# Kernel tuning notes

Hardware: AMD Instinct MI355X
Metric: run time of the kernel (lower is better)

Reference implementation:

```python
import jax, jax.numpy as jnp
import numpy as np

N_EMBD = 1024
N_HEAD = 16
HEAD_DIM = N_EMBD // N_HEAD


def setup_inputs() -> dict:
    key = jax.random.key(0)
    ks = jax.random.split(key, 5)
    scale = 0.02
    x = jax.random.normal(ks[0], (2, 2048, N_EMBD), dtype=jnp.float32)
    w_attn = jax.random.normal(ks[1], (N_EMBD, 3 * N_EMBD), dtype=jnp.float32) * scale
    b_attn = jax.random.normal(ks[2], (3 * N_EMBD,), dtype=jnp.float32) * scale
    w_proj = jax.random.normal(ks[3], (N_EMBD, N_EMBD), dtype=jnp.float32) * scale
    b_proj = jax.random.normal(ks[4], (N_EMBD,), dtype=jnp.float32) * scale
    return {"x": x, "w_attn": w_attn, "b_attn": b_attn, "w_proj": w_proj, "b_proj": b_proj}


def reference(x, w_attn, b_attn, w_proj, b_proj):
    B, T, C = x.shape
    qkv = x @ w_attn + b_attn  # [B,T,3C]
    q, k, v = jnp.split(qkv, 3, axis=-1)
    # [B, H, T, D]
    q = q.reshape(B, T, N_HEAD, HEAD_DIM).transpose(0, 2, 1, 3)
    k = k.reshape(B, T, N_HEAD, HEAD_DIM).transpose(0, 2, 1, 3)
    v = v.reshape(B, T, N_HEAD, HEAD_DIM).transpose(0, 2, 1, 3)
    att = jnp.einsum("bhqd,bhkd->bhqk", q, k) * (1.0 / np.sqrt(HEAD_DIM))
    causal = jnp.tril(jnp.ones((T, T), dtype=bool))
    att = jnp.where(causal[None, None], att, jnp.float32(-jnp.inf))
    att = jax.nn.softmax(att, axis=-1)
    y = jnp.einsum("bhqk,bhkd->bhqd", att, v)  # [B,H,T,D]
    y = y.transpose(0, 2, 1, 3).reshape(B, T, C)
    return y @ w_proj + b_proj
```

## Files before the change

kernel.cpp:

```cpp
#include <hip/hip_runtime.h>
#include <stdint.h>

#define SEQ   2048
#define EMBD  1024
#define M_ROWS 4096

typedef unsigned short u16;
typedef unsigned int u32;
typedef __attribute__((ext_vector_type(8))) short bf16x8;
typedef __attribute__((ext_vector_type(4))) float f32x4;

__device__ __forceinline__ u16 f2b(float f) {
  u32 x = __float_as_uint(f);
  return (u16)((x + 0x7FFFu + ((x >> 16) & 1u)) >> 16);
}

#define AS1(p) ((const __attribute__((address_space(1))) void*)(uintptr_t)(p))
#define AS3(p) ((__attribute__((address_space(3))) void*)(uintptr_t)(p))

__global__ __launch_bounds__(256) void cvt_f32_bf16(
    const float* __restrict__ in, u16* __restrict__ out, int n8) {
  int i = blockIdx.x * 256 + threadIdx.x;
  if (i >= n8) return;
  const float4* p = (const float4*)in + 2 * (size_t)i;
  float4 a = p[0], b = p[1];
  uint4 o;
  o.x = (u32)f2b(a.x) | ((u32)f2b(a.y) << 16);
  o.y = (u32)f2b(a.z) | ((u32)f2b(a.w) << 16);
  o.z = (u32)f2b(b.x) | ((u32)f2b(b.y) << 16);
  o.w = (u32)f2b(b.z) | ((u32)f2b(b.w) << 16);
  ((uint4*)out)[i] = o;
}

__global__ __launch_bounds__(256) void transpose_cvt(
    const float* __restrict__ w, u16* __restrict__ wt, int K, int N) {
  __shared__ float t[64][65];
  const int n0 = blockIdx.x * 64, k0 = blockIdx.y * 64;
  const int c = threadIdx.x & 63, r4 = threadIdx.x >> 6;
#pragma unroll
  for (int j = 0; j < 16; ++j) {
    const int r = j * 4 + r4;
    t[c][r] = w[(size_t)(k0 + r) * N + n0 + c];
  }
  __syncthreads();
#pragma unroll
  for (int j = 0; j < 16; ++j) {
    const int nr = j * 4 + r4;
    wt[(size_t)(n0 + nr) * K + k0 + c] = f2b(t[nr][c]);
  }
}

template <bool OUT_BF16>
__global__ __launch_bounds__(256) void gemm_kmajor(
    const u16* __restrict__ A, const u16* __restrict__ Bt,
    const float* __restrict__ bias, void* __restrict__ outp,
    int M, int N, int K, int nbx) {
  __shared__ __align__(16) u16 As[128 * 32];
  __shared__ __align__(16) u16 Bs[128 * 32];

  const int nwg = gridDim.x;
  const int qq = nwg >> 3, rr = nwg & 7;
  const int xcd = blockIdx.x & 7, off = blockIdx.x >> 3;
  const int wgid = (xcd < rr ? xcd * (qq + 1) : rr * (qq + 1) + (xcd - rr) * qq) + off;
  const int bx = wgid % nbx, by = wgid / nbx;
  const int row0 = by * 128, col0 = bx * 128;

  const int tid = threadIdx.x;
  const int w = tid >> 6, lane = tid & 63;
  const int wrow = (w >> 1) * 64, wcol = (w & 1) * 64;

  f32x4 acc[4][4];
#pragma unroll
  for (int a = 0; a < 4; ++a)
#pragma unroll
    for (int b = 0; b < 4; ++b)
#pragma unroll
      for (int e = 0; e < 4; ++e) acc[a][b][e] = 0.f;

  const size_t Kb = (size_t)K * 2;

  for (int k0 = 0; k0 < K; k0 += 32) {
#pragma unroll
    for (int c = 0; c < 4; ++c) {
      const int ch = w * 4 + c;
      const int i = ch & 7;
      const int rloc = i * 16 + (lane >> 2);
      const int kb = ((lane & 3) * 16) ^ ((rloc & 3) << 4);
      const char* src;
      char* dst;
      if (ch < 8) {
        src = (const char*)A + (size_t)(row0 + rloc) * Kb + k0 * 2 + kb;
        dst = (char*)As + i * 1024;
      } else {
        src = (const char*)Bt + (size_t)(col0 + rloc) * Kb + k0 * 2 + kb;
        dst = (char*)Bs + i * 1024;
      }
      __builtin_amdgcn_global_load_lds(AS1(src), AS3(dst), 16, 0, 0);
    }
    __syncthreads();

    bf16x8 af[4], bf[4];
#pragma unroll
    for (int rb = 0; rb < 4; ++rb) {
      const int rl = wrow + rb * 16 + (lane & 15);
      const int kb2 = ((lane >> 4) * 16) ^ ((rl & 3) << 4);
      af[rb] = *(const bf16x8*)((const char*)As + rl * 64 + kb2);
    }
#pragma unroll
    for (int cb = 0; cb < 4; ++cb) {
      const int rl = wcol + cb * 16 + (lane & 15);
      const int kb2 = ((lane >> 4) * 16) ^ ((rl & 3) << 4);
      bf[cb] = *(const bf16x8*)((const char*)Bs + rl * 64 + kb2);
    }
#pragma unroll
    for (int rb = 0; rb < 4; ++rb)
#pragma unroll
      for (int cb = 0; cb < 4; ++cb)
        acc[rb][cb] = __builtin_amdgcn_mfma_f32_16x16x32_bf16(
            af[rb], bf[cb], acc[rb][cb], 0, 0, 0);
    __syncthreads();
  }

#pragma unroll
  for (int cb = 0; cb < 4; ++cb) {
    const int colg = col0 + wcol + cb * 16 + (lane & 15);
    const float bv = bias[colg];
#pragma unroll
    for (int rb = 0; rb < 4; ++rb) {
#pragma unroll
      for (int i = 0; i < 4; ++i) {
        const int rowg = row0 + wrow + rb * 16 + (lane >> 4) * 4 + i;
        const float v = acc[rb][cb][i] + bv;
        if (OUT_BF16) {
          const u32 hv = f2b(v);
          const u32 pv = (u32)__shfl_xor((int)hv, 1);
          if (!(lane & 1))
            *(u32*)((u16*)outp + (size_t)rowg * N + colg) = hv | (pv << 16);
        } else {
          ((float*)outp)[(size_t)rowg * N + colg] = v;
        }
      }
    }
  }
}

__global__ __launch_bounds__(256) void attn_mfma(
    const u16* __restrict__ qkvb, u16* __restrict__ yb) {
  __shared__ __align__(16) u16 Ks[64 * 64];
  __shared__ __align__(16) u16 Vt[64 * 64];
  __shared__ __align__(16) u16 Ps[4][16 * 64];

  const int bx = blockIdx.x;
  const int qt = 31 - (bx >> 5);
  const int bh = bx & 31;
  const int bb = bh >> 4, h = bh & 15;

  const int tid = threadIdx.x;
  const int w = tid >> 6, lane = tid & 63;

  const size_t rowb = 3072 * 2;
  const char* base = (const char*)qkvb + (size_t)bb * SEQ * rowb;
  const int qoffb = h * 128;
  const int koffb = EMBD * 2 + h * 128;
  const int voffb = 2 * EMBD * 2 + h * 128;

  bf16x8 qf[2];
  {
    const int qrow = qt * 64 + w * 16 + (lane & 15);
    const char* qp = base + (size_t)qrow * rowb + qoffb + (lane >> 4) * 16;
    qf[0] = *(const bf16x8*)(qp);
    qf[1] = *(const bf16x8*)(qp + 64);
  }

  float mreg[4], lreg[4];
  f32x4 of[4];
#pragma unroll
  for (int i = 0; i < 4; ++i) {
    mreg[i] = -1e30f;
    lreg[i] = 0.f;
#pragma unroll
    for (int e = 0; e < 4; ++e) of[i][e] = 0.f;
  }

  const int vkv = tid & 63, vdb = tid >> 6;

  for (int kt = 0; kt <= qt; ++kt) {
#pragma unroll
    for (int c = 0; c < 2; ++c) {
      const int i = w * 2 + c;
      const int kv = i * 8 + (lane >> 3);
      const int db = ((lane & 7) * 16) ^ ((kv & 7) << 4);
      const char* src = base + (size_t)(kt * 64 + kv) * rowb + koffb + db;
      __builtin_amdgcn_global_load_lds(AS1(src), AS3((char*)Ks + i * 1024), 16, 0, 0);
    }
    {
      const char* vp = base + (size_t)(kt * 64 + vkv) * rowb + voffb + vdb * 32;
      union { uint4 q4[2]; u16 hh[16]; } vv;
      vv.q4[0] = *(const uint4*)vp;
      vv.q4[1] = *(const uint4*)(vp + 16);
#pragma unroll
      for (int e = 0; e < 16; ++e) {
        const int d = vdb * 16 + e;
        Vt[d * 64 + (vkv ^ ((d & 7) << 3))] = vv.hh[e];
      }
    }
    __syncthreads();

    f32x4 s[4];
#pragma unroll
    for (int cb = 0; cb < 4; ++cb)
#pragma unroll
      for (int e = 0; e < 4; ++e) s[cb][e] = 0.f;
#pragma unroll
    for (int cb = 0; cb < 4; ++cb) {
      const int kv = cb * 16 + (lane & 15);
      const int swz = (kv & 7) << 4;
      const char* kp = (const char*)Ks + kv * 128;
      bf16x8 kf0 = *(const bf16x8*)(kp + (((lane >> 4) * 16) ^ swz));
      bf16x8 kf1 = *(const bf16x8*)(kp + ((64 + (lane >> 4) * 16) ^ swz));
      s[cb] = __builtin_amdgcn_mfma_f32_16x16x32_bf16(qf[0], kf0, s[cb], 0, 0, 0);
      s[cb] = __builtin_amdgcn_mfma_f32_16x16x32_bf16(qf[1], kf1, s[cb], 0, 0, 0);
    }

    const int qg0 = qt * 64 + w * 16 + (lane >> 4) * 4;
    const int kvg0 = kt * 64 + (lane & 15);
    float pmax[4] = {-1e30f, -1e30f, -1e30f, -1e30f};
#pragma unroll
    for (int cb = 0; cb < 4; ++cb)
#pragma unroll
      for (int i = 0; i < 4; ++i) {
        float v = s[cb][i] * 0.125f;
        if (kvg0 + cb * 16 > qg0 + i) v = -1e30f;
        s[cb][i] = v;
        pmax[i] = fmaxf(pmax[i], v);
      }
#pragma unroll
    for (int i = 0; i < 4; ++i) {
      pmax[i] = fmaxf(pmax[i], __shfl_xor(pmax[i], 1));
      pmax[i] = fmaxf(pmax[i], __shfl_xor(pmax[i], 2));
      pmax[i] = fmaxf(pmax[i], __shfl_xor(pmax[i], 4));
      pmax[i] = fmaxf(pmax[i], __shfl_xor(pmax[i], 8));
    }
    float alpha[4], rsum[4];
#pragma unroll
    for (int i = 0; i < 4; ++i) {
      const float mn = fmaxf(mreg[i], pmax[i]);
      alpha[i] = __expf(mreg[i] - mn);
      mreg[i] = mn;
      rsum[i] = 0.f;
    }
#pragma unroll
    for (int cb = 0; cb < 4; ++cb)
#pragma unroll
      for (int i = 0; i < 4; ++i) {
        const float p = __expf(s[cb][i] - mreg[i]);
        rsum[i] += p;
        const int prow = (lane >> 4) * 4 + i;
        const int pcol = cb * 16 + (lane & 15);
        Ps[w][prow * 64 + (pcol ^ ((prow & 7) << 3))] = f2b(p);
      }
#pragma unroll
    for (int i = 0; i < 4; ++i) {
      rsum[i] += __shfl_xor(rsum[i], 1);
      rsum[i] += __shfl_xor(rsum[i], 2);
      rsum[i] += __shfl_xor(rsum[i], 4);
      rsum[i] += __shfl_xor(rsum[i], 8);
      lreg[i] = lreg[i] * alpha[i] + rsum[i];
    }
#pragma unroll
    for (int db = 0; db < 4; ++db)
#pragma unroll
      for (int i = 0; i < 4; ++i) of[db][i] *= alpha[i];

    bf16x8 pa[2];
    {
      const int prow = lane & 15;
      const int swz = (prow & 7) << 3;
      pa[0] = *(const bf16x8*)(&Ps[w][prow * 64 + ((8 * (lane >> 4)) ^ swz)]);
      pa[1] = *(const bf16x8*)(&Ps[w][prow * 64 + ((8 * (lane >> 4) + 32) ^ swz)]);
    }
#pragma unroll
    for (int db = 0; db < 4; ++db) {
      const int d = db * 16 + (lane & 15);
      const int swz = (d & 7) << 3;
      const u16* vp = &Vt[d * 64];
      bf16x8 v0 = *(const bf16x8*)(vp + ((8 * (lane >> 4)) ^ swz));
      bf16x8 v1 = *(const bf16x8*)(vp + ((8 * (lane >> 4) + 32) ^ swz));
      of[db] = __builtin_amdgcn_mfma_f32_16x16x32_bf16(pa[0], v0, of[db], 0, 0, 0);
      of[db] = __builtin_amdgcn_mfma_f32_16x16x32_bf16(pa[1], v1, of[db], 0, 0, 0);
    }
    __syncthreads();
  }

#pragma unroll
  for (int i = 0; i < 4; ++i) lreg[i] = 1.f / lreg[i];
  const int qrow0 = qt * 64 + w * 16 + (lane >> 4) * 4;
#pragma unroll
  for (int db = 0; db < 4; ++db) {
    const int colb = h * 64 + db * 16 + (lane & 15);
#pragma unroll
    for (int i = 0; i < 4; ++i) {
      const float v = of[db][i] * lreg[i];
      yb[(size_t)(bb * SEQ + qrow0 + i) * EMBD + colb] = f2b(v);
    }
  }
}

extern "C" void kernel_launch(void* const* d_in, const int* in_sizes, int n_in,
                              void* d_out, int out_size, void* d_ws,
                              size_t ws_size, hipStream_t stream) {
  const float* x      = (const float*)d_in[0];
  const float* w_attn = (const float*)d_in[1];
  const float* b_attn = (const float*)d_in[2];
  const float* w_proj = (const float*)d_in[3];
  const float* b_proj = (const float*)d_in[4];
  float* out = (float*)d_out;

  u16* xb   = (u16*)d_ws;
  u16* wat  = xb + (size_t)M_ROWS * EMBD;
  u16* wpt  = wat + (size_t)3 * EMBD * EMBD;
  u16* qkvb = wpt + (size_t)EMBD * EMBD;
  u16* yb   = qkvb + (size_t)M_ROWS * 3 * EMBD;

  cvt_f32_bf16<<<(M_ROWS * EMBD / 8 + 255) / 256, 256, 0, stream>>>(
      x, xb, M_ROWS * EMBD / 8);
  transpose_cvt<<<dim3(3 * EMBD / 64, EMBD / 64), 256, 0, stream>>>(
      w_attn, wat, EMBD, 3 * EMBD);
  transpose_cvt<<<dim3(EMBD / 64, EMBD / 64), 256, 0, stream>>>(
      w_proj, wpt, EMBD, EMBD);

  gemm_kmajor<true><<<768, 256, 0, stream>>>(
      xb, wat, b_attn, qkvb, M_ROWS, 3 * EMBD, EMBD, 24);

  attn_mfma<<<1024, 256, 0, stream>>>(qkvb, yb);

  gemm_kmajor<false><<<256, 256, 0, stream>>>(
      yb, wpt, b_proj, out, M_ROWS, EMBD, EMBD, 8);
}
```

Measured before the change: 227.3 us.

## Rewrite attention kernel with paired query tiles, double-buffered K/V, transposed S

Each attention block now handles two complementary query tiles (qt and 31-qt), which balances causal work across 512 blocks. K and V tiles are double-buffered in LDS, so the next tile's loads are issued while the current tile is computed. S is computed transposed (K as the A operand), so P can be packed into registers with v_cvt_pk_bf16_f32 instead of taking an LDS round trip. Softmax switches to exp2 with a folded scale, applies the mask only on the diagonal tile, and rescales lazily, skipping the rescale unless the max grows by more than a threshold. The cost is more complex code and larger LDS use, with a risk of lower occupancy.

```diff
diff --git a/kernel.cpp b/kernel.cpp
--- a/kernel.cpp
+++ b/kernel.cpp
@@ -13,6 +13,28 @@
 __device__ __forceinline__ u16 f2b(float f) {
   u32 x = __float_as_uint(f);
   return (u16)((x + 0x7FFFu + ((x >> 16) & 1u)) >> 16);
+}
+
+__device__ __forceinline__ u32 pkbf(float a, float b) {
+  u32 r;
+  asm("v_cvt_pk_bf16_f32 %0, %1, %2" : "=v"(r) : "v"(a), "v"(b));
+  return r;
+}
+
+__device__ __forceinline__ float exp2fast(float x) {
+#if __has_builtin(__builtin_amdgcn_exp2f)
+  return __builtin_amdgcn_exp2f(x);
+#else
+  return __expf(x * 0.69314718f);
+#endif
+}
+
+__device__ __forceinline__ float rcpfast(float x) {
+#if __has_builtin(__builtin_amdgcn_rcpf)
+  return __builtin_amdgcn_rcpf(x);
+#else
+  return 1.f / x;
+#endif
 }
 
 #define AS1(p) ((const __attribute__((address_space(1))) void*)(uintptr_t)(p))
@@ -144,165 +166,203 @@
   }
 }
 
-__global__ __launch_bounds__(256) void attn_mfma(
+__global__ __launch_bounds__(256, 2) void attn_mfma2(
     const u16* __restrict__ qkvb, u16* __restrict__ yb) {
-  __shared__ __align__(16) u16 Ks[64 * 64];
-  __shared__ __align__(16) u16 Vt[64 * 64];
-  __shared__ __align__(16) u16 Ps[4][16 * 64];
+  __shared__ __align__(16) char lds[32768];
 
   const int bx = blockIdx.x;
-  const int qt = 31 - (bx >> 5);
+  const int pr = bx >> 5;
   const int bh = bx & 31;
   const int bb = bh >> 4, h = bh & 15;
 
   const int tid = threadIdx.x;
   const int w = tid >> 6, lane = tid & 63;
-
-  const size_t rowb = 3072 * 2;
+  const int hh = lane >> 4, qh = lane & 15;
+
+  const size_t rowb = 6144;
   const char* base = (const char*)qkvb + (size_t)bb * SEQ * rowb;
-  const int qoffb = h * 128;
   const int koffb = EMBD * 2 + h * 128;
   const int voffb = 2 * EMBD * 2 + h * 128;
 
-  bf16x8 qf[2];
-  {
-    const int qrow = qt * 64 + w * 16 + (lane & 15);
-    const char* qp = base + (size_t)qrow * rowb + qoffb + (lane >> 4) * 16;
-    qf[0] = *(const bf16x8*)(qp);
-    qf[1] = *(const bf16x8*)(qp + 64);
-  }
-
-  float mreg[4], lreg[4];
-  f32x4 of[4];
-#pragma unroll
-  for (int i = 0; i < 4; ++i) {
-    mreg[i] = -1e30f;
-    lreg[i] = 0.f;
-#pragma unroll
-    for (int e = 0; e < 4; ++e) of[i][e] = 0.f;
-  }
-
-  const int vkv = tid & 63, vdb = tid >> 6;
-
-  for (int kt = 0; kt <= qt; ++kt) {
-#pragma unroll
-    for (int c = 0; c < 2; ++c) {
-      const int i = w * 2 + c;
-      const int kv = i * 8 + (lane >> 3);
-      const int db = ((lane & 7) * 16) ^ ((kv & 7) << 4);
-      const char* src = base + (size_t)(kt * 64 + kv) * rowb + koffb + db;
-      __builtin_amdgcn_global_load_lds(AS1(src), AS3((char*)Ks + i * 1024), 16, 0, 0);
-    }
+  const int krow_in_chunk = lane >> 3;
+  const int vkv = (tid & 31) * 2;
+  const int vdg = tid >> 5;
+
+  for (int half = 0; half < 2; ++half) {
+    const int qt = half ? pr : 31 - pr;
+    const int q_abs = qt * 64 + w * 16 + qh;
+    const int qloc = w * 16 + qh;
+
+    const char* qp = base + (size_t)q_abs * rowb + h * 128 + hh * 16;
+    const bf16x8 qf0 = *(const bf16x8*)qp;
+    const bf16x8 qf1 = *(const bf16x8*)(qp + 64);
+
+    float m2 = -1e30f, l = 0.f;
+    f32x4 of[4];
+#pragma unroll
+    for (int db = 0; db < 4; ++db)
+#pragma unroll
+      for (int e = 0; e < 4; ++e) of[db][e] = 0.f;
+
     {
-      const char* vp = base + (size_t)(kt * 64 + vkv) * rowb + voffb + vdb * 32;
-      union { uint4 q4[2]; u16 hh[16]; } vv;
-      vv.q4[0] = *(const uint4*)vp;
-      vv.q4[1] = *(const uint4*)(vp + 16);
-#pragma unroll
-      for (int e = 0; e < 16; ++e) {
-        const int d = vdb * 16 + e;
-        Vt[d * 64 + (vkv ^ ((d & 7) << 3))] = vv.hh[e];
+#pragma unroll
+      for (int cc = 0; cc < 2; ++cc) {
+        const int i = w * 2 + cc;
+        const int kvl = i * 8 + krow_in_chunk;
+        const int gs = (lane & 7) ^ ((i & 3) | ((krow_in_chunk & 1) << 2));
+        const char* src = base + (size_t)kvl * rowb + koffb + gs * 16;
+        __builtin_amdgcn_global_load_lds(AS1(src), AS3(lds + i * 1024), 16, 0, 0);
+      }
+      const char* vp = base + (size_t)vkv * rowb + voffb + vdg * 16;
+      uint4 va = *(const uint4*)vp;
+      uint4 vb = *(const uint4*)(vp + rowb);
+      union { uint4 q; u16 s[8]; } ua, ub;
+      ua.q = va; ub.q = vb;
+      u32* vt = (u32*)(lds + 16384);
+#pragma unroll
+      for (int e = 0; e < 8; ++e) {
+        const int d = vdg * 8 + e;
+        vt[d * 32 + ((vkv >> 1) ^ ((d & 7) << 2))] =
+            (u32)ua.s[e] | ((u32)ub.s[e] << 16);
       }
     }
     __syncthreads();
 
-    f32x4 s[4];
-#pragma unroll
-    for (int cb = 0; cb < 4; ++cb)
-#pragma unroll
-      for (int e = 0; e < 4; ++e) s[cb][e] = 0.f;
-#pragma unroll
-    for (int cb = 0; cb < 4; ++cb) {
-      const int kv = cb * 16 + (lane & 15);
-      const int swz = (kv & 7) << 4;
-      const char* kp = (const char*)Ks + kv * 128;
-      bf16x8 kf0 = *(const bf16x8*)(kp + (((lane >> 4) * 16) ^ swz));
-      bf16x8 kf1 = *(const bf16x8*)(kp + ((64 + (lane >> 4) * 16) ^ swz));
-      s[cb] = __builtin_amdgcn_mfma_f32_16x16x32_bf16(qf[0], kf0, s[cb], 0, 0, 0);
-      s[cb] = __builtin_amdgcn_mfma_f32_16x16x32_bf16(qf[1], kf1, s[cb], 0, 0, 0);
-    }
-
-    const int qg0 = qt * 64 + w * 16 + (lane >> 4) * 4;
-    const int kvg0 = kt * 64 + (lane & 15);
-    float pmax[4] = {-1e30f, -1e30f, -1e30f, -1e30f};
-#pragma unroll
-    for (int cb = 0; cb < 4; ++cb)
-#pragma unroll
-      for (int i = 0; i < 4; ++i) {
-        float v = s[cb][i] * 0.125f;
-        if (kvg0 + cb * 16 > qg0 + i) v = -1e30f;
-        s[cb][i] = v;
-        pmax[i] = fmaxf(pmax[i], v);
-      }
-#pragma unroll
-    for (int i = 0; i < 4; ++i) {
-      pmax[i] = fmaxf(pmax[i], __shfl_xor(pmax[i], 1));
-      pmax[i] = fmaxf(pmax[i], __shfl_xor(pmax[i], 2));
-      pmax[i] = fmaxf(pmax[i], __shfl_xor(pmax[i], 4));
-      pmax[i] = fmaxf(pmax[i], __shfl_xor(pmax[i], 8));
-    }
-    float alpha[4], rsum[4];
-#pragma unroll
-    for (int i = 0; i < 4; ++i) {
-      const float mn = fmaxf(mreg[i], pmax[i]);
-      alpha[i] = __expf(mreg[i] - mn);
-      mreg[i] = mn;
-      rsum[i] = 0.f;
-    }
-#pragma unroll
-    for (int cb = 0; cb < 4; ++cb)
-#pragma unroll
-      for (int i = 0; i < 4; ++i) {
-        const float p = __expf(s[cb][i] - mreg[i]);
-        rsum[i] += p;
-        const int prow = (lane >> 4) * 4 + i;
-        const int pcol = cb * 16 + (lane & 15);
-        Ps[w][prow * 64 + (pcol ^ ((prow & 7) << 3))] = f2b(p);
-      }
-#pragma unroll
-    for (int i = 0; i < 4; ++i) {
-      rsum[i] += __shfl_xor(rsum[i], 1);
-      rsum[i] += __shfl_xor(rsum[i], 2);
-      rsum[i] += __shfl_xor(rsum[i], 4);
-      rsum[i] += __shfl_xor(rsum[i], 8);
-      lreg[i] = lreg[i] * alpha[i] + rsum[i];
-    }
-#pragma unroll
-    for (int db = 0; db < 4; ++db)
-#pragma unroll
-      for (int i = 0; i < 4; ++i) of[db][i] *= alpha[i];
-
-    bf16x8 pa[2];
-    {
-      const int prow = lane & 15;
-      const int swz = (prow & 7) << 3;
-      pa[0] = *(const bf16x8*)(&Ps[w][prow * 64 + ((8 * (lane >> 4)) ^ swz)]);
-      pa[1] = *(const bf16x8*)(&Ps[w][prow * 64 + ((8 * (lane >> 4) + 32) ^ swz)]);
-    }
+    for (int kt = 0; kt <= qt; ++kt) {
+      const int cur = kt & 1;
+      const char* ksb = lds + cur * 8192;
+      const char* vtb = lds + 16384 + cur * 8192;
+
+      uint4 va, vb;
+      const bool pref = (kt < qt);
+      if (pref) {
+#pragma unroll
+        for (int cc = 0; cc < 2; ++cc) {
+          const int i = w * 2 + cc;
+          const int kvl = i * 8 + krow_in_chunk;
+          const int gs = (lane & 7) ^ ((i & 3) | ((krow_in_chunk & 1) << 2));
+          const char* src =
+              base + (size_t)((kt + 1) * 64 + kvl) * rowb + koffb + gs * 16;
+          __builtin_amdgcn_global_load_lds(
+              AS1(src), AS3(lds + (cur ^ 1) * 8192 + i * 1024), 16, 0, 0);
+        }
+        const char* vp =
+            base + (size_t)((kt + 1) * 64 + vkv) * rowb + voffb + vdg * 16;
+        va = *(const uint4*)vp;
+        vb = *(const uint4*)(vp + rowb);
+      }
+
+      f32x4 st[4];
+#pragma unroll
+      for (int rb = 0; rb < 4; ++rb) {
+#pragma unroll
+        for (int e = 0; e < 4; ++e) st[rb][e] = 0.f;
+        const int kv = 32 * (rb >> 1) + 8 * ((lane >> 2) & 3) + 4 * (rb & 1) +
+                       (lane & 3);
+        const int f = ((kv >> 3) & 3) | ((kv & 1) << 2);
+        const char* rp = ksb + kv * 128;
+        const bf16x8 k0 = *(const bf16x8*)(rp + ((hh * 16) ^ (f << 4)));
+        const bf16x8 k1 = *(const bf16x8*)(rp + ((64 + hh * 16) ^ (f << 4)));
+        st[rb] = __builtin_amdgcn_mfma_f32_16x16x32_bf16(k0, qf0, st[rb], 0, 0, 0);
+        st[rb] = __builtin_amdgcn_mfma_f32_16x16x32_bf16(k1, qf1, st[rb], 0, 0, 0);
+      }
+
+      const float C = 0.18033688f;
+      float pmax = -3.0e38f;
+      if (kt == qt) {
+#pragma unroll
+        for (int rb = 0; rb < 4; ++rb) {
+          const int kvb = 32 * (rb >> 1) + 8 * hh + 4 * (rb & 1);
+#pragma unroll
+          for (int i = 0; i < 4; ++i) {
+            float v = st[rb][i] * C;
+            if (kvb + i > qloc) v = -3.0e38f;
+            st[rb][i] = v;
+            pmax = fmaxf(pmax, v);
+          }
+        }
+      } else {
+#pragma unroll
+        for (int rb = 0; rb < 4; ++rb)
+#pragma unroll
+          for (int i = 0; i < 4; ++i) {
+            const float v = st[rb][i] * C;
+            st[rb][i] = v;
+            pmax = fmaxf(pmax, v);
+          }
+      }
+      pmax = fmaxf(pmax, __shfl_xor(pmax, 16));
+      pmax = fmaxf(pmax, __shfl_xor(pmax, 32));
+
+      if (__any(pmax > m2 + 5.f)) {
+        const float mn = fmaxf(m2, pmax);
+        const float al = exp2fast(m2 - mn);
+        m2 = mn;
+        l *= al;
+#pragma unroll
+        for (int db = 0; db < 4; ++db)
+#pragma unroll
+          for (int e = 0; e < 4; ++e) of[db][e] *= al;
+      }
+
+      float ls = 0.f;
+#pragma unroll
+      for (int rb = 0; rb < 4; ++rb)
+#pragma unroll
+        for (int i = 0; i < 4; ++i) {
+          const float p = exp2fast(st[rb][i] - m2);
+          st[rb][i] = p;
+          ls += p;
+        }
+      ls += __shfl_xor(ls, 16);
+      ls += __shfl_xor(ls, 32);
+      l += ls;
+
+      union { u32 wd[4]; bf16x8 v; } pf0, pf1;
+      pf0.wd[0] = pkbf(st[0][0], st[0][1]);
+      pf0.wd[1] = pkbf(st[0][2], st[0][3]);
+      pf0.wd[2] = pkbf(st[1][0], st[1][1]);
+      pf0.wd[3] = pkbf(st[1][2], st[1][3]);
+      pf1.wd[0] = pkbf(st[2][0], st[2][1]);
+      pf1.wd[1] = pkbf(st[2][2], st[2][3]);
+      pf1.wd[2] = pkbf(st[3][0], st[3][1]);
+      pf1.wd[3] = pkbf(st[3][2], st[3][3]);
+
+#pragma unroll
+      for (int db = 0; db < 4; ++db) {
+        const int d = db * 16 + qh;
+        const int g = d & 7;
+        const char* rp = vtb + d * 128;
+        const bf16x8 v0 = *(const bf16x8*)(rp + ((hh * 16) ^ (g << 4)));
+        const bf16x8 v1 = *(const bf16x8*)(rp + ((64 + hh * 16) ^ (g << 4)));
+        of[db] = __builtin_amdgcn_mfma_f32_16x16x32_bf16(v0, pf0.v, of[db], 0, 0, 0);
+        of[db] = __builtin_amdgcn_mfma_f32_16x16x32_bf16(v1, pf1.v, of[db], 0, 0, 0);
+      }
+
+      if (pref) {
+        union { uint4 q; u16 s[8]; } ua, ub;
+        ua.q = va; ub.q = vb;
+        u32* vt = (u32*)(lds + 16384 + (cur ^ 1) * 8192);
+#pragma unroll
+        for (int e = 0; e < 8; ++e) {
+          const int d = vdg * 8 + e;
+          vt[d * 32 + ((vkv >> 1) ^ ((d & 7) << 2))] =
+              (u32)ua.s[e] | ((u32)ub.s[e] << 16);
+        }
+      }
+      __syncthreads();
+    }
+
+    const float inv = rcpfast(l);
+    u16* yrow = yb + (size_t)(bb * SEQ + q_abs) * EMBD + h * 64;
 #pragma unroll
     for (int db = 0; db < 4; ++db) {
-      const int d = db * 16 + (lane & 15);
-      const int swz = (d & 7) << 3;
-      const u16* vp = &Vt[d * 64];
-      bf16x8 v0 = *(const bf16x8*)(vp + ((8 * (lane >> 4)) ^ swz));
-      bf16x8 v1 = *(const bf16x8*)(vp + ((8 * (lane >> 4) + 32) ^ swz));
-      of[db] = __builtin_amdgcn_mfma_f32_16x16x32_bf16(pa[0], v0, of[db], 0, 0, 0);
-      of[db] = __builtin_amdgcn_mfma_f32_16x16x32_bf16(pa[1], v1, of[db], 0, 0, 0);
+      const u32 w0 = pkbf(of[db][0] * inv, of[db][1] * inv);
+      const u32 w1 = pkbf(of[db][2] * inv, of[db][3] * inv);
+      *(u32*)(yrow + db * 16 + 4 * hh) = w0;
+      *(u32*)(yrow + db * 16 + 4 * hh + 2) = w1;
     }
     __syncthreads();
-  }
-
-#pragma unroll
-  for (int i = 0; i < 4; ++i) lreg[i] = 1.f / lreg[i];
-  const int qrow0 = qt * 64 + w * 16 + (lane >> 4) * 4;
-#pragma unroll
-  for (int db = 0; db < 4; ++db) {
-    const int colb = h * 64 + db * 16 + (lane & 15);
-#pragma unroll
-    for (int i = 0; i < 4; ++i) {
-      const float v = of[db][i] * lreg[i];
-      yb[(size_t)(bb * SEQ + qrow0 + i) * EMBD + colb] = f2b(v);
-    }
   }
 }
 
@@ -332,7 +392,7 @@
   gemm_kmajor<true><<<768, 256, 0, stream>>>(
       xb, wat, b_attn, qkvb, M_ROWS, 3 * EMBD, EMBD, 24);
 
-  attn_mfma<<<1024, 256, 0, stream>>>(qkvb, yb);
+  attn_mfma2<<<512, 256, 0, stream>>>(qkvb, yb);
 
   gemm_kmajor<false><<<256, 256, 0, stream>>>(
       yb, wpt, b_proj, out, M_ROWS, EMBD, EMBD, 8);
```

After: 207.7 us. 8.7% less time.
